# Performance work log

Hardware: AMD Instinct MI355X
Metric: run time of the kernel (lower is better)

The kernel has to match this reference:

```python
import jax, jax.numpy as jnp
import numpy as np

T_VID = 129  # TACoS iou grid size

def make_iou_mask_map():
    m = np.zeros((129, 129), np.float32)
    for i in range(0, 128):
        m[i, 1 + i:min(i + 17, 129)] = 1.0
    for i in range(0, 128 - 16, 2):
        m[i, list(range(18 + i, min(33 + i, 129), 2))] = 1.0
    for i in range(0, 128 - 32, 4):
        m[i, list(range(36 + i, min(65 + i, 129), 4))] = 1.0
    for i in range(0, 128 - 64, 8):
        m[i, list(range(72 + i, 129, 8))] = 1.0
    return jnp.asarray(m)

def setup_inputs() -> dict:
    key = jax.random.key(0)
    B, L, T, D, CH, V = 8, 100, T_VID, 512, 512, 1000
    ks = jax.random.split(key, 20)
    g = lambda k, shp, fan: jax.random.normal(k, shp, jnp.float32) * (1.0 / np.sqrt(fan))
    return {
        'hidden_states_text': jax.random.normal(ks[0], (B, L, D), jnp.float32),
        'hidden_states_object': jax.random.normal(ks[1], (B, T, D), jnp.float32),
        # final_mlp (text head): D->CH->V
        'w_t1': g(ks[2], (D, CH), D), 'b_t1': jnp.zeros((CH,), jnp.float32),
        'w_t2': g(ks[3], (CH, V), CH), 'b_t2': jnp.zeros((V,), jnp.float32),
        # final_mlp_2: D -> 3D (+ReLU)
        'w2': g(ks[4], (D, 3 * D), D), 'b2': jnp.zeros((3 * D,), jnp.float32),
        # final_mlp_3: 3D -> CH -> 3
        'w3a': g(ks[5], (3 * D, CH), 3 * D), 'b3a': jnp.zeros((CH,), jnp.float32),
        'w3b': g(ks[6], (CH, 3), CH), 'b3b': jnp.zeros((3,), jnp.float32),
        # final_mlp_s/e/c: D -> CH -> 1
        'w_s1': g(ks[7], (D, CH), D), 'b_s1': jnp.zeros((CH,), jnp.float32),
        'w_s2': g(ks[8], (CH, 1), CH), 'b_s2': jnp.zeros((1,), jnp.float32),
        'w_e1': g(ks[9], (D, CH), D), 'b_e1': jnp.zeros((CH,), jnp.float32),
        'w_e2': g(ks[10], (CH, 1), CH), 'b_e2': jnp.zeros((1,), jnp.float32),
        'w_c1': g(ks[11], (D, CH), D), 'b_c1': jnp.zeros((CH,), jnp.float32),
        'w_c2': g(ks[12], (CH, 1), CH), 'b_c2': jnp.zeros((1,), jnp.float32),
    }

def _head(x, w1, b1, w2, b2):
    return jax.nn.relu(x @ w1 + b1) @ w2 + b2

def reference(hidden_states_text, hidden_states_object,
              w_t1, b_t1, w_t2, b_t2, w2, b2, w3a, b3a, w3b, b3b,
              w_s1, b_s1, w_s2, b_s2, w_e1, b_e1, w_e2, b_e2,
              w_c1, b_c1, w_c2, b_c2):
    D = hidden_states_object.shape[-1]
    T = hidden_states_object.shape[1]
    # text head (dropout is identity at inference)
    logits_text = _head(hidden_states_text, w_t1, b_t1, w_t2, b_t2)
    # final_mlp_2 then split into start/center/end streams, each [B,T,D]
    h = jax.nn.relu(hidden_states_object @ w2 + b2)
    hs, hc, he = h[..., :D], h[..., D:2 * D], h[..., 2 * D:]
    # final_mlp_3 first linear decomposed over the concat blocks:
    # grid[b,i,j] = W_s.hs[i] + W_c.hc[(i+j)//2] + W_e.he[j] + b  (same math as
    # cat(repeat(hs), gather(hc), repeat(he)) @ w3a, without the 3D grid)
    ps = hc @ w3a[D:2 * D]            # [B,T,CH] (center projection, gathered below)
    pS = hs @ w3a[:D]                 # [B,T,CH]
    pE = he @ w3a[2 * D:]             # [B,T,CH]
    idx = (jnp.arange(T)[:, None] + jnp.arange(T)[None, :]) // 2  # [T,T] center index
    grid = pS[:, :, None, :] + ps[:, idx, :] + pE[:, None, :, :] + b3a  # [B,T,T,CH]
    logits_iou = (jax.nn.relu(grid) @ w3b + b3b)  # [B,T,T,3]
    logits_iou = jnp.transpose(logits_iou, (0, 3, 1, 2))  # [B,3,T,T]
    logits_visual = jnp.concatenate([
        _head(hs, w_s1, b_s1, w_s2, b_s2),
        _head(he, w_e1, b_e1, w_e2, b_e2),
        _head(hc, w_c1, b_c1, w_c2, b_c2)], axis=-1)  # [B,T,3]
    return logits_text, logits_visual, logits_iou, make_iou_mask_map()
```

## Files before the change

kernel.cpp:

```cpp
#include <hip/hip_runtime.h>
#include <hip/hip_bf16.h>

typedef unsigned short ushort_t;
typedef __attribute__((ext_vector_type(8))) short bf16x8;
typedef __attribute__((ext_vector_type(4))) float f32x4;

constexpr int BB = 8, LL = 100, TT = 129, DD = 512, CH = 512, VV = 1000;
constexpr int M_TXT = BB * LL;
constexpr int M_OBJ = BB * TT;
constexpr int P_SLAB = M_OBJ * DD;
constexpr int N_IOU = BB * 3 * TT * TT;
constexpr int N_VIS = 3 * M_OBJ;
constexpr int N_MASK = TT * TT;

constexpr int OUT_TEXT = 0;
constexpr int OUT_VIS  = M_TXT * VV;
constexpr int OUT_IOU  = OUT_VIS + N_VIS;
constexpr int OUT_MASK = OUT_IOU + N_IOU;

constexpr size_t WB_TEXT = 0;
constexpr size_t WB_OBJ  = WB_TEXT + 819200;
constexpr size_t WB_WT1  = WB_OBJ  + 1056768;
constexpr size_t WB_WT2  = WB_WT1  + 524288;
constexpr size_t WB_W2T  = WB_WT2  + 1024000;
constexpr size_t WB_W3AT = WB_W2T  + 1572864;
constexpr size_t WB_WS1T = WB_W3AT + 1572864;
constexpr size_t WB_WE1T = WB_WS1T + 524288;
constexpr size_t WB_WC1T = WB_WE1T + 524288;
constexpr size_t WB_T1   = WB_WC1T + 524288;
constexpr size_t WB_H    = WB_T1   + 819200;
constexpr size_t WB_P    = WB_H    + 3170304;
constexpr size_t WB_PART = WB_P    + 6340608;
constexpr size_t WB_IOUP = 0;

__device__ __forceinline__ ushort_t f2bf(float x) {
    __hip_bfloat16 h = __float2bfloat16(x);
    return *(ushort_t*)&h;
}

struct TDesc { const float* src; ushort_t* dst; int R, C, tiles, ctiles; };
struct PrepArgs {
    const float* act_a; ushort_t* act_da; int na4;
    const float* act_b; ushort_t* act_db; int nb4;
    int nact_blocks;
    TDesc t[7];
};

__global__ __launch_bounds__(256)
void prep_kernel(PrepArgs pa)
{
    if ((int)blockIdx.x < pa.nact_blocks) {
        int gid = blockIdx.x * 256 + threadIdx.x;
        const float* src; ushort_t* dst;
        if (gid < pa.na4) { src = pa.act_a + gid * 4; dst = pa.act_da + gid * 4; }
        else { gid -= pa.na4; if (gid >= pa.nb4) return; src = pa.act_b + gid * 4; dst = pa.act_db + gid * 4; }
        f32x4 v = *(const f32x4*)src;
        dst[0] = f2bf(v[0]); dst[1] = f2bf(v[1]); dst[2] = f2bf(v[2]); dst[3] = f2bf(v[3]);
        return;
    }
    __shared__ float tl[32][33];
    int bx = blockIdx.x - pa.nact_blocks;
    TDesc e;
    #pragma unroll
    for (int i = 0; i < 7; ++i) {
        if (bx < pa.t[i].tiles) { e = pa.t[i]; break; }
        bx -= pa.t[i].tiles;
    }
    const int tx = threadIdx.x & 31, ty = threadIdx.x >> 5;
    const int rt = bx / e.ctiles, ct = bx - rt * e.ctiles;
    #pragma unroll
    for (int i = 0; i < 4; ++i) {
        const int r = rt * 32 + ty + i * 8, c = ct * 32 + tx;
        tl[ty + i * 8][tx] = (r < e.R && c < e.C) ? e.src[(size_t)r * e.C + c] : 0.0f;
    }
    __syncthreads();
    #pragma unroll
    for (int i = 0; i < 4; ++i) {
        const int dr = ct * 32 + ty + i * 8, dc = rt * 32 + tx;
        if (dr < e.C && dc < e.R)
            e.dst[(size_t)dr * e.R + dc] = f2bf(tl[tx][ty + i * 8]);
    }
}

struct GemmDesc {
    const ushort_t* A; int lda;
    const ushort_t* Bt; int ldb;
    const float* bias;
    void* C; int ldc;
    int M, N, K;
    int mode;
    const float* w2head;
    float* partial;
    int ntiles, ntx;
};
struct GemmArgs { GemmDesc d[7]; };

__global__ __launch_bounds__(256)
void gemm_mfma(GemmArgs args)
{
    int bx = blockIdx.x, zi = 0;
    while (bx >= args.d[zi].ntiles) { bx -= args.d[zi].ntiles; ++zi; }
    const GemmDesc g = args.d[zi];
    const int tyT = bx / g.ntx, txT = bx - tyT * g.ntx;
    const int m0 = tyT * 128, n0 = txT * 128;

    __shared__ ushort_t ldsA[2][128 * 32];
    __shared__ ushort_t ldsB[2][128 * 32];

    const int tid = threadIdx.x;
    const int w = tid >> 6, l = tid & 63;
    const int wr = w >> 1, wc = w & 1;

    const int srow = l >> 2;
    const int scol = (l & 3) << 3;
    const int wbase = w << 4;

    f32x4 acc[4][4];
    #pragma unroll
    for (int mi = 0; mi < 4; ++mi)
        #pragma unroll
        for (int ni = 0; ni < 4; ++ni)
            acc[mi][ni] = f32x4{0.f, 0.f, 0.f, 0.f};

    const int nk = g.K >> 5;

    auto stage = [&](int buf, int k0) {
        #pragma unroll
        for (int q = 0; q < 2; ++q) {
            int gm = m0 + (q << 6) + wbase + srow; if (gm >= g.M) gm = g.M - 1;
            __builtin_amdgcn_global_load_lds(
                (const __attribute__((address_space(1))) unsigned int*)(g.A + (size_t)gm * g.lda + k0 + scol),
                (__attribute__((address_space(3))) unsigned int*)&ldsA[buf][((q << 6) + wbase) * 32],
                16, 0, 0);
            int gn = n0 + (q << 6) + wbase + srow; if (gn >= g.N) gn = g.N - 1;
            __builtin_amdgcn_global_load_lds(
                (const __attribute__((address_space(1))) unsigned int*)(g.Bt + (size_t)gn * g.ldb + k0 + scol),
                (__attribute__((address_space(3))) unsigned int*)&ldsB[buf][((q << 6) + wbase) * 32],
                16, 0, 0);
        }
    };

    stage(0, 0);
    int cur = 0;
    const int fr = l & 15, kq = (l >> 4) << 3;

    for (int kt = 0; kt < nk; ++kt) {
        __syncthreads();
        if (kt + 1 < nk) stage(cur ^ 1, (kt + 1) << 5);
        bf16x8 av[4], bv[4];
        #pragma unroll
        for (int mi = 0; mi < 4; ++mi)
            av[mi] = *(const bf16x8*)&ldsA[cur][((wr << 6) + (mi << 4) + fr) * 32 + kq];
        #pragma unroll
        for (int ni = 0; ni < 4; ++ni)
            bv[ni] = *(const bf16x8*)&ldsB[cur][((wc << 6) + (ni << 4) + fr) * 32 + kq];
        #pragma unroll
        for (int mi = 0; mi < 4; ++mi)
            #pragma unroll
            for (int ni = 0; ni < 4; ++ni)
                acc[mi][ni] = __builtin_amdgcn_mfma_f32_16x16x32_bf16(av[mi], bv[ni], acc[mi][ni], 0, 0, 0);
        cur ^= 1;
    }

    const int rq = (l >> 4) << 2;
    if (g.mode == 2) {
        float s[4][4];
        #pragma unroll
        for (int mi = 0; mi < 4; ++mi)
            #pragma unroll
            for (int r = 0; r < 4; ++r) s[mi][r] = 0.f;
        #pragma unroll
        for (int ni = 0; ni < 4; ++ni) {
            const int col = n0 + (wc << 6) + (ni << 4) + fr;
            const float bb = g.bias[col];
            const float wv = g.w2head[col];
            #pragma unroll
            for (int mi = 0; mi < 4; ++mi)
                #pragma unroll
                for (int r = 0; r < 4; ++r) {
                    float v = fmaxf(acc[mi][ni][r] + bb, 0.f);
                    s[mi][r] = fmaf(v, wv, s[mi][r]);
                }
        }
        #pragma unroll
        for (int off = 1; off < 16; off <<= 1)
            #pragma unroll
            for (int mi = 0; mi < 4; ++mi)
                #pragma unroll
                for (int r = 0; r < 4; ++r)
                    s[mi][r] += __shfl_xor(s[mi][r], off);
        if (fr == 0) {
            const int chunk = txT * 2 + wc;
            #pragma unroll
            for (int mi = 0; mi < 4; ++mi)
                #pragma unroll
                for (int r = 0; r < 4; ++r) {
                    const int row = m0 + (wr << 6) + (mi << 4) + rq + r;
                    if (row < g.M) g.partial[row * 8 + chunk] = s[mi][r];
                }
        }
    } else {
        #pragma unroll
        for (int ni = 0; ni < 4; ++ni) {
            const int col = n0 + (wc << 6) + (ni << 4) + fr;
            const float bb = (g.bias && col < g.N) ? g.bias[col] : 0.f;
            #pragma unroll
            for (int mi = 0; mi < 4; ++mi)
                #pragma unroll
                for (int r = 0; r < 4; ++r) {
                    const int row = m0 + (wr << 6) + (mi << 4) + rq + r;
                    if (row < g.M && col < g.N) {
                        float v = acc[mi][ni][r] + bb;
                        if (g.mode == 1) {
                            v = fmaxf(v, 0.f);
                            ((ushort_t*)g.C)[(size_t)row * g.ldc + col] = f2bf(v);
                        } else {
                            ((float*)g.C)[(size_t)row * g.ldc + col] = v;
                        }
                    }
                }
        }
    }
}

__global__ __launch_bounds__(256)
void iou_partial_kernel(const float* __restrict__ P, const float* __restrict__ w3b,
                        float* __restrict__ iop)
{
    __shared__ __align__(16) float sP[96 * 132];
    __shared__ __align__(16) float sW[384];

    const int tid = threadIdx.x;
    const int b = blockIdx.z >> 2;
    const int cs = blockIdx.z & 3;
    const int c0 = cs << 7;
    const int i0 = blockIdx.y * 32, j0 = blockIdx.x * 32;
    const int idx0 = (i0 + j0) >> 1;
    const int par = (i0 + j0) & 1;

    for (int f = tid; f < 384; f += 256) {
        const int k = f >> 7, c = f & 127;
        sW[f] = w3b[(c0 + c) * 3 + k];
    }
    for (int f = tid; f < 3072; f += 256) {
        const int row = f >> 5;
        const int pos = (f & 31) << 2;
        const int a = row >> 5;
        const int r = row & 31;
        int rg = (a == 0) ? (i0 + r) : (a == 1) ? (idx0 + r) : (j0 + r);
        if (rg > 128) rg = 128;
        f32x4 v = *(const f32x4*)&P[(size_t)a * P_SLAB + ((size_t)(b * TT) + rg) * DD + c0 + pos];
        *(f32x4*)&sP[row * 132 + pos] = v;
    }
    __syncthreads();

    const int ii = tid >> 4, jj = tid & 15;
    const int o = ((ii + jj + par) >> 1) + 32;
    float a00[3] = {0,0,0}, a01[3] = {0,0,0}, a10[3] = {0,0,0}, a11[3] = {0,0,0};

    const float* rs0 = &sP[ii * 132];
    const float* rs1 = &sP[(ii + 16) * 132];
    const float* rp0 = &sP[o * 132];
    const float* rp1 = &sP[(o + 8) * 132];
    const float* rp2 = &sP[(o + 16) * 132];
    const float* re0 = &sP[(64 + jj) * 132];
    const float* re1 = &sP[(64 + jj + 16) * 132];

    #pragma unroll 4
    for (int c = 0; c < 128; c += 4) {
        const f32x4 s0 = *(const f32x4*)&rs0[c];
        const f32x4 s1 = *(const f32x4*)&rs1[c];
        const f32x4 p0 = *(const f32x4*)&rp0[c];
        const f32x4 p1 = *(const f32x4*)&rp1[c];
        const f32x4 p2 = *(const f32x4*)&rp2[c];
        const f32x4 e0 = *(const f32x4*)&re0[c];
        const f32x4 e1 = *(const f32x4*)&re1[c];
        const f32x4 w0 = *(const f32x4*)&sW[c];
        const f32x4 w1 = *(const f32x4*)&sW[128 + c];
        const f32x4 w2 = *(const f32x4*)&sW[256 + c];
        #pragma unroll
        for (int u = 0; u < 4; ++u) {
            const float v00 = fmaxf(s0[u] + p0[u] + e0[u], 0.f);
            const float v01 = fmaxf(s0[u] + p1[u] + e1[u], 0.f);
            const float v10 = fmaxf(s1[u] + p1[u] + e0[u], 0.f);
            const float v11 = fmaxf(s1[u] + p2[u] + e1[u], 0.f);
            a00[0] = fmaf(v00, w0[u], a00[0]); a00[1] = fmaf(v00, w1[u], a00[1]); a00[2] = fmaf(v00, w2[u], a00[2]);
            a01[0] = fmaf(v01, w0[u], a01[0]); a01[1] = fmaf(v01, w1[u], a01[1]); a01[2] = fmaf(v01, w2[u], a01[2]);
            a10[0] = fmaf(v10, w0[u], a10[0]); a10[1] = fmaf(v10, w1[u], a10[1]); a10[2] = fmaf(v10, w2[u], a10[2]);
            a11[0] = fmaf(v11, w0[u], a11[0]); a11[1] = fmaf(v11, w1[u], a11[1]); a11[2] = fmaf(v11, w2[u], a11[2]);
        }
    }

    float* dst = iop + (size_t)cs * N_IOU;
    auto emit = [&](const float* acc, int i, int j) {
        if (i <= 128 && j <= 128) {
            #pragma unroll
            for (int k = 0; k < 3; ++k)
                dst[((size_t)(b * 3 + k) * TT + i) * TT + j] = acc[k];
        }
    };
    emit(a00, i0 + ii, j0 + jj);
    emit(a01, i0 + ii, j0 + jj + 16);
    emit(a10, i0 + ii + 16, j0 + jj);
    emit(a11, i0 + ii + 16, j0 + jj + 16);
}

__global__ __launch_bounds__(256)
void finalize_kernel(const float* __restrict__ iop, const float* __restrict__ part,
                     const float* __restrict__ b3b,
                     const float* __restrict__ bs2, const float* __restrict__ be2,
                     const float* __restrict__ bc2,
                     float* __restrict__ out)
{
    int g = blockIdx.x * 256 + threadIdx.x;
    if (g < N_IOU) {
        const int bk = g / (TT * TT);
        const int k = bk - (bk / 3) * 3;
        const float s = iop[g] + iop[N_IOU + g] + iop[2 * N_IOU + g] + iop[3 * N_IOU + g];
        out[OUT_IOU + g] = s + b3b[k];
        return;
    }
    g -= N_IOU;
    if (g < N_VIS) {
        const int head = g / M_OBJ;
        const int row = g - head * M_OBJ;
        const float* p = part + (size_t)(head * M_OBJ + row) * 8;
        float s = 0.f;
        #pragma unroll
        for (int c = 0; c < 8; ++c) s += p[c];
        const float bias = head == 0 ? bs2[0] : (head == 1 ? be2[0] : bc2[0]);
        out[OUT_VIS + row * 3 + head] = s + bias;
        return;
    }
    g -= N_VIS;
    if (g < N_MASK) {
        const int i = g / TT, j = g - i * TT;
        const int d = j - i;
        bool v = false;
        if (i < 128 && d >= 1 && d <= 16) v = true;
        if (!v && (i & 1) == 0 && i <= 110 && d >= 18 && d <= 32 && (d & 1) == 0) v = true;
        if (!v && (i & 3) == 0 && i <= 92  && d >= 36 && d <= 64 && (d & 3) == 0) v = true;
        if (!v && (i & 7) == 0 && i <= 56  && d >= 72 && (d & 7) == 0) v = true;
        out[OUT_MASK + g] = v ? 1.0f : 0.0f;
    }
}

extern "C" void kernel_launch(void* const* d_in, const int* in_sizes, int n_in,
                              void* d_out, int out_size, void* d_ws, size_t ws_size,
                              hipStream_t stream)
{
    const float* text = (const float*)d_in[0];
    const float* obj  = (const float*)d_in[1];
    const float* w_t1 = (const float*)d_in[2];
    const float* b_t1 = (const float*)d_in[3];
    const float* w_t2 = (const float*)d_in[4];
    const float* b_t2 = (const float*)d_in[5];
    const float* w2   = (const float*)d_in[6];
    const float* b2   = (const float*)d_in[7];
    const float* w3a  = (const float*)d_in[8];
    const float* b3a  = (const float*)d_in[9];
    const float* w3b  = (const float*)d_in[10];
    const float* b3b  = (const float*)d_in[11];
    const float* w_s1 = (const float*)d_in[12];
    const float* b_s1 = (const float*)d_in[13];
    const float* w_s2 = (const float*)d_in[14];
    const float* b_s2 = (const float*)d_in[15];
    const float* w_e1 = (const float*)d_in[16];
    const float* b_e1 = (const float*)d_in[17];
    const float* w_e2 = (const float*)d_in[18];
    const float* b_e2 = (const float*)d_in[19];
    const float* w_c1 = (const float*)d_in[20];
    const float* b_c1 = (const float*)d_in[21];
    const float* w_c2 = (const float*)d_in[22];
    const float* b_c2 = (const float*)d_in[23];

    float* out = (float*)d_out;
    char* ws = (char*)d_ws;
    ushort_t* text_bf = (ushort_t*)(ws + WB_TEXT);
    ushort_t* obj_bf  = (ushort_t*)(ws + WB_OBJ);
    ushort_t* wt1     = (ushort_t*)(ws + WB_WT1);
    ushort_t* wt2     = (ushort_t*)(ws + WB_WT2);
    ushort_t* w2t     = (ushort_t*)(ws + WB_W2T);
    ushort_t* w3at    = (ushort_t*)(ws + WB_W3AT);
    ushort_t* ws1t    = (ushort_t*)(ws + WB_WS1T);
    ushort_t* we1t    = (ushort_t*)(ws + WB_WE1T);
    ushort_t* wc1t    = (ushort_t*)(ws + WB_WC1T);
    ushort_t* T1      = (ushort_t*)(ws + WB_T1);
    ushort_t* H       = (ushort_t*)(ws + WB_H);
    float*    P       = (float*)(ws + WB_P);
    float*    part    = (float*)(ws + WB_PART);
    float*    iop     = (float*)(ws + WB_IOUP);

    {
        PrepArgs pa;
        pa.act_a = text; pa.act_da = text_bf; pa.na4 = (M_TXT * DD) / 4;
        pa.act_b = obj;  pa.act_db = obj_bf;  pa.nb4 = (M_OBJ * DD) / 4;
        pa.nact_blocks = (pa.na4 + pa.nb4 + 255) / 256;
        pa.t[0] = {w_t1, wt1, 512, 512, 256, 16};
        pa.t[1] = {w_t2, wt2, 512, 1000, 512, 32};
        pa.t[2] = {w2, w2t, 512, 1536, 768, 48};
        pa.t[3] = {w3a, w3at, 1536, 512, 768, 16};
        pa.t[4] = {w_s1, ws1t, 512, 512, 256, 16};
        pa.t[5] = {w_e1, we1t, 512, 512, 256, 16};
        pa.t[6] = {w_c1, wc1t, 512, 512, 256, 16};
        prep_kernel<<<dim3(pa.nact_blocks + 3072), dim3(256), 0, stream>>>(pa);
    }
    {
        GemmArgs a{};
        a.d[0] = {text_bf, DD, wt1, DD, b_t1, T1, CH, M_TXT, CH, DD, 1, nullptr, nullptr, 28, 4};
        a.d[1] = {obj_bf, DD, w2t, DD, b2, H, 3 * DD, M_OBJ, 3 * DD, DD, 1, nullptr, nullptr, 108, 12};
        gemm_mfma<<<dim3(136), dim3(256), 0, stream>>>(a);
    }
    {
        GemmArgs a{};
        a.d[0] = {T1, CH, wt2, CH, b_t2, out + OUT_TEXT, VV, M_TXT, VV, CH, 0, nullptr, nullptr, 56, 8};
        a.d[1] = {H + 0 * DD, 3 * DD, w3at + 0 * DD, 3 * DD, b3a, P + 0 * P_SLAB, DD, M_OBJ, DD, DD, 0, nullptr, nullptr, 36, 4};
        a.d[2] = {H + 1 * DD, 3 * DD, w3at + 1 * DD, 3 * DD, nullptr, P + 1 * P_SLAB, DD, M_OBJ, DD, DD, 0, nullptr, nullptr, 36, 4};
        a.d[3] = {H + 2 * DD, 3 * DD, w3at + 2 * DD, 3 * DD, nullptr, P + 2 * P_SLAB, DD, M_OBJ, DD, DD, 0, nullptr, nullptr, 36, 4};
        a.d[4] = {H + 0 * DD, 3 * DD, ws1t, DD, b_s1, nullptr, 0, M_OBJ, CH, DD, 2, w_s2, part + 0 * M_OBJ * 8, 36, 4};
        a.d[5] = {H + 2 * DD, 3 * DD, we1t, DD, b_e1, nullptr, 0, M_OBJ, CH, DD, 2, w_e2, part + 1 * M_OBJ * 8, 36, 4};
        a.d[6] = {H + 1 * DD, 3 * DD, wc1t, DD, b_c1, nullptr, 0, M_OBJ, CH, DD, 2, w_c2, part + 2 * M_OBJ * 8, 36, 4};
        gemm_mfma<<<dim3(272), dim3(256), 0, stream>>>(a);
    }
    iou_partial_kernel<<<dim3(5, 5, 32), dim3(256), 0, stream>>>(P, w3b, iop);
    finalize_kernel<<<dim3((N_IOU + N_VIS + N_MASK + 255) / 256), dim3(256), 0, stream>>>(
        iop, part, b3b, b_s2, b_e2, b_c2, out);
}
```

Baseline: 87.44 us.

## Remove finalize kernel; reduce IoU and visual partials with atomics into bias-initialized output

The output is now seeded with the biases and the mask map inside the prep kernel. The IoU kernel and the visual-head GEMM epilogue add their partial sums straight into the output with atomicAdd. This drops the finalize launch and the partial buffers that had to be written to and read back from the workspace. The IoU inner loop is also rewritten with f32x4 vector max and FMA operations. Atomic contention is small (4 channel slices per IoU element), but floating-point summation order is now nondeterministic.

```diff
diff --git a/kernel.cpp b/kernel.cpp
--- a/kernel.cpp
+++ b/kernel.cpp
@@ -30,8 +30,6 @@
 constexpr size_t WB_T1   = WB_WC1T + 524288;
 constexpr size_t WB_H    = WB_T1   + 819200;
 constexpr size_t WB_P    = WB_H    + 3170304;
-constexpr size_t WB_PART = WB_P    + 6340608;
-constexpr size_t WB_IOUP = 0;
 
 __device__ __forceinline__ ushort_t f2bf(float x) {
     __hip_bfloat16 h = __float2bfloat16(x);
@@ -42,15 +40,18 @@
 struct PrepArgs {
     const float* act_a; ushort_t* act_da; int na4;
     const float* act_b; ushort_t* act_db; int nb4;
-    int nact_blocks;
+    int nact_blocks, nwt_blocks;
     TDesc t[7];
+    const float *b3b, *bs2, *be2, *bc2;
+    float* out;
 };
 
 __global__ __launch_bounds__(256)
 void prep_kernel(PrepArgs pa)
 {
-    if ((int)blockIdx.x < pa.nact_blocks) {
-        int gid = blockIdx.x * 256 + threadIdx.x;
+    const int bxg = blockIdx.x;
+    if (bxg < pa.nact_blocks) {
+        int gid = bxg * 256 + threadIdx.x;
         const float* src; ushort_t* dst;
         if (gid < pa.na4) { src = pa.act_a + gid * 4; dst = pa.act_da + gid * 4; }
         else { gid -= pa.na4; if (gid >= pa.nb4) return; src = pa.act_b + gid * 4; dst = pa.act_db + gid * 4; }
@@ -58,27 +59,55 @@
         dst[0] = f2bf(v[0]); dst[1] = f2bf(v[1]); dst[2] = f2bf(v[2]); dst[3] = f2bf(v[3]);
         return;
     }
-    __shared__ float tl[32][33];
-    int bx = blockIdx.x - pa.nact_blocks;
-    TDesc e;
-    #pragma unroll
-    for (int i = 0; i < 7; ++i) {
-        if (bx < pa.t[i].tiles) { e = pa.t[i]; break; }
-        bx -= pa.t[i].tiles;
-    }
-    const int tx = threadIdx.x & 31, ty = threadIdx.x >> 5;
-    const int rt = bx / e.ctiles, ct = bx - rt * e.ctiles;
-    #pragma unroll
-    for (int i = 0; i < 4; ++i) {
-        const int r = rt * 32 + ty + i * 8, c = ct * 32 + tx;
-        tl[ty + i * 8][tx] = (r < e.R && c < e.C) ? e.src[(size_t)r * e.C + c] : 0.0f;
-    }
-    __syncthreads();
-    #pragma unroll
-    for (int i = 0; i < 4; ++i) {
-        const int dr = ct * 32 + ty + i * 8, dc = rt * 32 + tx;
-        if (dr < e.C && dc < e.R)
-            e.dst[(size_t)dr * e.R + dc] = f2bf(tl[tx][ty + i * 8]);
+    if (bxg < pa.nact_blocks + pa.nwt_blocks) {
+        __shared__ float tl[32][33];
+        int bx = bxg - pa.nact_blocks;
+        TDesc e;
+        #pragma unroll
+        for (int i = 0; i < 7; ++i) {
+            if (bx < pa.t[i].tiles) { e = pa.t[i]; break; }
+            bx -= pa.t[i].tiles;
+        }
+        const int tx = threadIdx.x & 31, ty = threadIdx.x >> 5;
+        const int rt = bx / e.ctiles, ct = bx - rt * e.ctiles;
+        #pragma unroll
+        for (int i = 0; i < 4; ++i) {
+            const int r = rt * 32 + ty + i * 8, c = ct * 32 + tx;
+            tl[ty + i * 8][tx] = (r < e.R && c < e.C) ? e.src[(size_t)r * e.C + c] : 0.0f;
+        }
+        __syncthreads();
+        #pragma unroll
+        for (int i = 0; i < 4; ++i) {
+            const int dr = ct * 32 + ty + i * 8, dc = rt * 32 + tx;
+            if (dr < e.C && dc < e.R)
+                e.dst[(size_t)dr * e.R + dc] = f2bf(tl[tx][ty + i * 8]);
+        }
+        return;
+    }
+    int g = (bxg - pa.nact_blocks - pa.nwt_blocks) * 256 + threadIdx.x;
+    if (g < N_IOU) {
+        const int bk = g / (TT * TT);
+        const int k = bk - (bk / 3) * 3;
+        pa.out[OUT_IOU + g] = pa.b3b[k];
+        return;
+    }
+    g -= N_IOU;
+    if (g < N_VIS) {
+        const int head = g - (g / 3) * 3;
+        const float bias = head == 0 ? pa.bs2[0] : (head == 1 ? pa.be2[0] : pa.bc2[0]);
+        pa.out[OUT_VIS + g] = bias;
+        return;
+    }
+    g -= N_VIS;
+    if (g < N_MASK) {
+        const int i = g / TT, j = g - i * TT;
+        const int d = j - i;
+        bool v = false;
+        if (i < 128 && d >= 1 && d <= 16) v = true;
+        if (!v && (i & 1) == 0 && i <= 110 && d >= 18 && d <= 32 && (d & 1) == 0) v = true;
+        if (!v && (i & 3) == 0 && i <= 92  && d >= 36 && d <= 64 && (d & 3) == 0) v = true;
+        if (!v && (i & 7) == 0 && i <= 56  && d >= 72 && (d & 7) == 0) v = true;
+        pa.out[OUT_MASK + g] = v ? 1.0f : 0.0f;
     }
 }
 
@@ -90,7 +119,8 @@
     int M, N, K;
     int mode;
     const float* w2head;
-    float* partial;
+    float* vbase;
+    int vhead;
     int ntiles, ntx;
 };
 struct GemmArgs { GemmDesc d[7]; };
@@ -190,13 +220,12 @@
                 for (int r = 0; r < 4; ++r)
                     s[mi][r] += __shfl_xor(s[mi][r], off);
         if (fr == 0) {
-            const int chunk = txT * 2 + wc;
             #pragma unroll
             for (int mi = 0; mi < 4; ++mi)
                 #pragma unroll
                 for (int r = 0; r < 4; ++r) {
                     const int row = m0 + (wr << 6) + (mi << 4) + rq + r;
-                    if (row < g.M) g.partial[row * 8 + chunk] = s[mi][r];
+                    if (row < g.M) atomicAdd(&g.vbase[row * 3 + g.vhead], s[mi][r]);
                 }
         }
     } else {
@@ -224,8 +253,8 @@
 }
 
 __global__ __launch_bounds__(256)
-void iou_partial_kernel(const float* __restrict__ P, const float* __restrict__ w3b,
-                        float* __restrict__ iop)
+void iou_kernel(const float* __restrict__ P, const float* __restrict__ w3b,
+                float* __restrict__ out)
 {
     __shared__ __align__(16) float sP[96 * 132];
     __shared__ __align__(16) float sW[384];
@@ -256,7 +285,6 @@
 
     const int ii = tid >> 4, jj = tid & 15;
     const int o = ((ii + jj + par) >> 1) + 32;
-    float a00[3] = {0,0,0}, a01[3] = {0,0,0}, a10[3] = {0,0,0}, a11[3] = {0,0,0};
 
     const float* rs0 = &sP[ii * 132];
     const float* rs1 = &sP[(ii + 16) * 132];
@@ -266,7 +294,12 @@
     const float* re0 = &sP[(64 + jj) * 132];
     const float* re1 = &sP[(64 + jj + 16) * 132];
 
-    #pragma unroll 4
+    const f32x4 z4 = {0.f, 0.f, 0.f, 0.f};
+    f32x4 av00[3], av01[3], av10[3], av11[3];
+    #pragma unroll
+    for (int k = 0; k < 3; ++k) { av00[k] = z4; av01[k] = z4; av10[k] = z4; av11[k] = z4; }
+
+    #pragma unroll 2
     for (int c = 0; c < 128; c += 4) {
         const f32x4 s0 = *(const f32x4*)&rs0[c];
         const f32x4 s1 = *(const f32x4*)&rs1[c];
@@ -278,71 +311,40 @@
         const f32x4 w0 = *(const f32x4*)&sW[c];
         const f32x4 w1 = *(const f32x4*)&sW[128 + c];
         const f32x4 w2 = *(const f32x4*)&sW[256 + c];
-        #pragma unroll
-        for (int u = 0; u < 4; ++u) {
-            const float v00 = fmaxf(s0[u] + p0[u] + e0[u], 0.f);
-            const float v01 = fmaxf(s0[u] + p1[u] + e1[u], 0.f);
-            const float v10 = fmaxf(s1[u] + p1[u] + e0[u], 0.f);
-            const float v11 = fmaxf(s1[u] + p2[u] + e1[u], 0.f);
-            a00[0] = fmaf(v00, w0[u], a00[0]); a00[1] = fmaf(v00, w1[u], a00[1]); a00[2] = fmaf(v00, w2[u], a00[2]);
-            a01[0] = fmaf(v01, w0[u], a01[0]); a01[1] = fmaf(v01, w1[u], a01[1]); a01[2] = fmaf(v01, w2[u], a01[2]);
-            a10[0] = fmaf(v10, w0[u], a10[0]); a10[1] = fmaf(v10, w1[u], a10[1]); a10[2] = fmaf(v10, w2[u], a10[2]);
-            a11[0] = fmaf(v11, w0[u], a11[0]); a11[1] = fmaf(v11, w1[u], a11[1]); a11[2] = fmaf(v11, w2[u], a11[2]);
-        }
-    }
-
-    float* dst = iop + (size_t)cs * N_IOU;
-    auto emit = [&](const float* acc, int i, int j) {
+
+        const f32x4 t00 = s0 + e0, t01 = s0 + e1, t10 = s1 + e0, t11 = s1 + e1;
+        const f32x4 v00 = __builtin_elementwise_max(t00 + p0, z4);
+        const f32x4 v01 = __builtin_elementwise_max(t01 + p1, z4);
+        const f32x4 v10 = __builtin_elementwise_max(t10 + p1, z4);
+        const f32x4 v11 = __builtin_elementwise_max(t11 + p2, z4);
+
+        av00[0] = __builtin_elementwise_fma(v00, w0, av00[0]);
+        av00[1] = __builtin_elementwise_fma(v00, w1, av00[1]);
+        av00[2] = __builtin_elementwise_fma(v00, w2, av00[2]);
+        av01[0] = __builtin_elementwise_fma(v01, w0, av01[0]);
+        av01[1] = __builtin_elementwise_fma(v01, w1, av01[1]);
+        av01[2] = __builtin_elementwise_fma(v01, w2, av01[2]);
+        av10[0] = __builtin_elementwise_fma(v10, w0, av10[0]);
+        av10[1] = __builtin_elementwise_fma(v10, w1, av10[1]);
+        av10[2] = __builtin_elementwise_fma(v10, w2, av10[2]);
+        av11[0] = __builtin_elementwise_fma(v11, w0, av11[0]);
+        av11[1] = __builtin_elementwise_fma(v11, w1, av11[1]);
+        av11[2] = __builtin_elementwise_fma(v11, w2, av11[2]);
+    }
+
+    auto emit = [&](const f32x4* acc, int i, int j) {
         if (i <= 128 && j <= 128) {
             #pragma unroll
-            for (int k = 0; k < 3; ++k)
-                dst[((size_t)(b * 3 + k) * TT + i) * TT + j] = acc[k];
+            for (int k = 0; k < 3; ++k) {
+                const float s = acc[k][0] + acc[k][1] + acc[k][2] + acc[k][3];
+                atomicAdd(&out[OUT_IOU + ((size_t)(b * 3 + k) * TT + i) * TT + j], s);
+            }
         }
     };
-    emit(a00, i0 + ii, j0 + jj);
-    emit(a01, i0 + ii, j0 + jj + 16);
-    emit(a10, i0 + ii + 16, j0 + jj);
-    emit(a11, i0 + ii + 16, j0 + jj + 16);
-}
-
-__global__ __launch_bounds__(256)
-void finalize_kernel(const float* __restrict__ iop, const float* __restrict__ part,
-                     const float* __restrict__ b3b,
-                     const float* __restrict__ bs2, const float* __restrict__ be2,
-                     const float* __restrict__ bc2,
-                     float* __restrict__ out)
-{
-    int g = blockIdx.x * 256 + threadIdx.x;
-    if (g < N_IOU) {
-        const int bk = g / (TT * TT);
-        const int k = bk - (bk / 3) * 3;
-        const float s = iop[g] + iop[N_IOU + g] + iop[2 * N_IOU + g] + iop[3 * N_IOU + g];
-        out[OUT_IOU + g] = s + b3b[k];
-        return;
-    }
-    g -= N_IOU;
-    if (g < N_VIS) {
-        const int head = g / M_OBJ;
-        const int row = g - head * M_OBJ;
-        const float* p = part + (size_t)(head * M_OBJ + row) * 8;
-        float s = 0.f;
-        #pragma unroll
-        for (int c = 0; c < 8; ++c) s += p[c];
-        const float bias = head == 0 ? bs2[0] : (head == 1 ? be2[0] : bc2[0]);
-        out[OUT_VIS + row * 3 + head] = s + bias;
-        return;
-    }
-    g -= N_VIS;
-    if (g < N_MASK) {
-        const int i = g / TT, j = g - i * TT;
-        const int d = j - i;
-        bool v = false;
-        if (i < 128 && d >= 1 && d <= 16) v = true;
-        if (!v && (i & 1) == 0 && i <= 110 && d >= 18 && d <= 32 && (d & 1) == 0) v = true;
-        if (!v && (i & 3) == 0 && i <= 92  && d >= 36 && d <= 64 && (d & 3) == 0) v = true;
-        if (!v && (i & 7) == 0 && i <= 56  && d >= 72 && (d & 7) == 0) v = true;
-        out[OUT_MASK + g] = v ? 1.0f : 0.0f;
-    }
+    emit(av00, i0 + ii, j0 + jj);
+    emit(av01, i0 + ii, j0 + jj + 16);
+    emit(av10, i0 + ii + 16, j0 + jj);
+    emit(av11, i0 + ii + 16, j0 + jj + 16);
 }
 
 extern "C" void kernel_launch(void* const* d_in, const int* in_sizes, int n_in,
@@ -388,14 +390,13 @@
     ushort_t* T1      = (ushort_t*)(ws + WB_T1);
     ushort_t* H       = (ushort_t*)(ws + WB_H);
     float*    P       = (float*)(ws + WB_P);
-    float*    part    = (float*)(ws + WB_PART);
-    float*    iop     = (float*)(ws + WB_IOUP);
 
     {
         PrepArgs pa;
         pa.act_a = text; pa.act_da = text_bf; pa.na4 = (M_TXT * DD) / 4;
         pa.act_b = obj;  pa.act_db = obj_bf;  pa.nb4 = (M_OBJ * DD) / 4;
         pa.nact_blocks = (pa.na4 + pa.nb4 + 255) / 256;
+        pa.nwt_blocks = 3072;
         pa.t[0] = {w_t1, wt1, 512, 512, 256, 16};
         pa.t[1] = {w_t2, wt2, 512, 1000, 512, 32};
         pa.t[2] = {w2, w2t, 512, 1536, 768, 48};
@@ -403,26 +404,27 @@
         pa.t[4] = {w_s1, ws1t, 512, 512, 256, 16};
         pa.t[5] = {w_e1, we1t, 512, 512, 256, 16};
         pa.t[6] = {w_c1, wc1t, 512, 512, 256, 16};
-        prep_kernel<<<dim3(pa.nact_blocks + 3072), dim3(256), 0, stream>>>(pa);
+        pa.b3b = b3b; pa.bs2 = b_s2; pa.be2 = b_e2; pa.bc2 = b_c2;
+        pa.out = out;
+        const int ninit = (N_IOU + N_VIS + N_MASK + 255) / 256;
+        prep_kernel<<<dim3(pa.nact_blocks + pa.nwt_blocks + ninit), dim3(256), 0, stream>>>(pa);
     }
     {
         GemmArgs a{};
-        a.d[0] = {text_bf, DD, wt1, DD, b_t1, T1, CH, M_TXT, CH, DD, 1, nullptr, nullptr, 28, 4};
-        a.d[1] = {obj_bf, DD, w2t, DD, b2, H, 3 * DD, M_OBJ, 3 * DD, DD, 1, nullptr, nullptr, 108, 12};
+        a.d[0] = {text_bf, DD, wt1, DD, b_t1, T1, CH, M_TXT, CH, DD, 1, nullptr, nullptr, 0, 28, 4};
+        a.d[1] = {obj_bf, DD, w2t, DD, b2, H, 3 * DD, M_OBJ, 3 * DD, DD, 1, nullptr, nullptr, 0, 108, 12};
         gemm_mfma<<<dim3(136), dim3(256), 0, stream>>>(a);
     }
     {
         GemmArgs a{};
-        a.d[0] = {T1, CH, wt2, CH, b_t2, out + OUT_TEXT, VV, M_TXT, VV, CH, 0, nullptr, nullptr, 56, 8};
-        a.d[1] = {H + 0 * DD, 3 * DD, w3at + 0 * DD, 3 * DD, b3a, P + 0 * P_SLAB, DD, M_OBJ, DD, DD, 0, nullptr, nullptr, 36, 4};
-        a.d[2] = {H + 1 * DD, 3 * DD, w3at + 1 * DD, 3 * DD, nullptr, P + 1 * P_SLAB, DD, M_OBJ, DD, DD, 0, nullptr, nullptr, 36, 4};
-        a.d[3] = {H + 2 * DD, 3 * DD, w3at + 2 * DD, 3 * DD, nullptr, P + 2 * P_SLAB, DD, M_OBJ, DD, DD, 0, nullptr, nullptr, 36, 4};
-        a.d[4] = {H + 0 * DD, 3 * DD, ws1t, DD, b_s1, nullptr, 0, M_OBJ, CH, DD, 2, w_s2, part + 0 * M_OBJ * 8, 36, 4};
-        a.d[5] = {H + 2 * DD, 3 * DD, we1t, DD, b_e1, nullptr, 0, M_OBJ, CH, DD, 2, w_e2, part + 1 * M_OBJ * 8, 36, 4};
-        a.d[6] = {H + 1 * DD, 3 * DD, wc1t, DD, b_c1, nullptr, 0, M_OBJ, CH, DD, 2, w_c2, part + 2 * M_OBJ * 8, 36, 4};
+        a.d[0] = {T1, CH, wt2, CH, b_t2, out + OUT_TEXT, VV, M_TXT, VV, CH, 0, nullptr, nullptr, 0, 56, 8};
+        a.d[1] = {H + 0 * DD, 3 * DD, w3at + 0 * DD, 3 * DD, b3a, P + 0 * P_SLAB, DD, M_OBJ, DD, DD, 0, nullptr, nullptr, 0, 36, 4};
+        a.d[2] = {H + 1 * DD, 3 * DD, w3at + 1 * DD, 3 * DD, nullptr, P + 1 * P_SLAB, DD, M_OBJ, DD, DD, 0, nullptr, nullptr, 0, 36, 4};
+        a.d[3] = {H + 2 * DD, 3 * DD, w3at + 2 * DD, 3 * DD, nullptr, P + 2 * P_SLAB, DD, M_OBJ, DD, DD, 0, nullptr, nullptr, 0, 36, 4};
+        a.d[4] = {H + 0 * DD, 3 * DD, ws1t, DD, b_s1, nullptr, 0, M_OBJ, CH, DD, 2, w_s2, out + OUT_VIS, 0, 36, 4};
+        a.d[5] = {H + 2 * DD, 3 * DD, we1t, DD, b_e1, nullptr, 0, M_OBJ, CH, DD, 2, w_e2, out + OUT_VIS, 1, 36, 4};
+        a.d[6] = {H + 1 * DD, 3 * DD, wc1t, DD, b_c1, nullptr, 0, M_OBJ, CH, DD, 2, w_c2, out + OUT_VIS, 2, 36, 4};
         gemm_mfma<<<dim3(272), dim3(256), 0, stream>>>(a);
     }
-    iou_partial_kernel<<<dim3(5, 5, 32), dim3(256), 0, stream>>>(P, w3b, iop);
-    finalize_kernel<<<dim3((N_IOU + N_VIS + N_MASK + 255) / 256), dim3(256), 0, stream>>>(
-        iop, part, b3b, b_s2, b_e2, b_c2, out);
+    iou_kernel<<<dim3(5, 5, 32), dim3(256), 0, stream>>>(P, w3b, out);
 }
```

New measurement: 87.46 us. Within noise of the previous version (+0.0%).
